# Performance work log

Hardware: AMD Instinct MI355X
Metric: run time of the kernel (lower is better)

## Reference

```python
import jax, jax.numpy as jnp
import numpy as np

M0, S0 = 0.0, 2.0       # normal prior mean / std on mu, beta
SHAPE, SCALE = 2.0, 1.0  # gamma prior on softplus(phi)


def _softplus(x):
    return jnp.logaddexp(x, 0.0)


def _log_negbinomial(y, mu, phi):
    # NB parameterized by mean mu and dispersion phi (var = mu + phi*mu^2)
    r = 1.0 / phi
    return (jax.lax.lgamma(y + r) - jax.lax.lgamma(r) - jax.lax.lgamma(y + 1.0)
            + r * jnp.log(r / (r + mu)) + y * jnp.log(mu / (r + mu)))


def _log_normal(x, m, s):
    return -0.5 * jnp.log(2.0 * jnp.pi * s * s) - (x - m) ** 2 / (2.0 * s * s)


def _log_gamma(x, shape, scale):
    return ((shape - 1.0) * jnp.log(x) - x / scale
            - jax.lax.lgamma(jnp.asarray(shape, x.dtype)) - shape * jnp.log(scale))


def setup_inputs() -> dict:
    key = jax.random.key(0)
    k1, k2, k3, k4, k5 = jax.random.split(key, 5)
    N, P, G = 1024, 4, 20000
    X = jax.random.normal(k1, (N, P), dtype=jnp.float32)
    Y = jax.random.randint(k2, (N, G), 0, 500).astype(jnp.float32)
    mu = jax.random.normal(k3, (G,), dtype=jnp.float32)
    beta = jax.random.normal(k4, (P * G,), dtype=jnp.float32)
    phi = jax.random.normal(k5, (G,), dtype=jnp.float32)
    return {"X": X, "Y": Y, "mu": mu, "beta": beta, "phi": phi}


def reference(X, Y, mu, beta, phi):
    N, P = X.shape
    G = Y.shape[1]
    beta_ = beta.reshape(P, G)
    log_unnorm = mu + X @ beta_                                   # [N, G]
    norm = jax.scipy.special.logsumexp(log_unnorm, axis=1, keepdims=True)
    pi = jnp.exp(log_unnorm - norm)                               # softmax over genes
    s = jnp.sum(Y, axis=1, keepdims=True)                         # [N, 1] library sizes
    phi_sp = _softplus(phi)                                       # [G]
    log_lik = jnp.sum(_log_negbinomial(Y, s * pi, phi_sp))
    log_prior = (jnp.sum(_log_normal(mu, M0, S0))
                 + jnp.sum(_log_normal(beta, M0, S0))
                 + jnp.sum(_log_gamma(phi_sp, SHAPE, SCALE)))
    return (log_lik + log_prior).reshape(1)
```

## Files before the change

kernel.cpp:

```cpp
#include <hip/hip_runtime.h>
#include <math.h>


#define RPB 16

__device__ __forceinline__ float fast_rcp(float x) {
    return __builtin_amdgcn_rcpf(x);
}

__device__ __forceinline__ float lgamma_pos(float x) {
    float lp = 0.0f;
    if (x < 8.0f) {
        float p = x;
        x += 1.0f;
        while (x < 8.0f) { p *= x; x += 1.0f; }
        lp = __logf(p);
    }
    float inv  = fast_rcp(x);
    float inv2 = inv * inv;
    float ser = inv * (0.08333333333f + inv2 * (-0.002777777778f + inv2 * 7.936507937e-4f));
    return (x - 0.5f) * __logf(x) - x + 0.9189385332f + ser - lp;
}

__device__ __forceinline__ float stirling_lg(float x) {
    float inv  = fast_rcp(x);
    float inv2 = inv * inv;
    float ser  = inv * (0.08333333333f - 0.002777777778f * inv2);
    return (x - 0.5f) * __logf(x) - x + 0.9189385332f + ser;
}

__device__ __forceinline__ float softplus_f(float x) {
    return fmaxf(x, 0.0f) + log1pf(__expf(-fabsf(x)));
}

__device__ __forceinline__ float wave_reduce(float v) {
#pragma unroll
    for (int off = 32; off; off >>= 1) v += __shfl_down(v, off, 64);
    return v;
}

__global__ __launch_bounds__(256) void setup_kernel(
        const float* __restrict__ mu, const float* __restrict__ beta,
        const float* __restrict__ phi, double* __restrict__ acc,
        float* __restrict__ rg, float* __restrict__ cgw, int P, int G) {
    int g = blockIdx.x * 256 + threadIdx.x;
    float v = 0.0f;
    if (g < G) {
        const float cn = -1.6120857137646180f;
        float m = mu[g];
        v = cn - m * m * 0.125f;
        for (int p = 0; p < P; ++p) {
            float b = beta[(size_t)p * G + g];
            v += cn - b * b * 0.125f;
        }
        float sp = softplus_f(phi[g]);
        v += __logf(sp) - sp;
        float r = 1.0f / sp;
        rg[g]  = r;
        cgw[g] = r * __logf(r) - lgamma_pos(r);
    }
    v = wave_reduce(v);
    __shared__ float red[4];
    int lane = threadIdx.x & 63, wid = threadIdx.x >> 6;
    if (lane == 0) red[wid] = v;
    __syncthreads();
    if (threadIdx.x == 0)
        atomicAdd(acc, (double)((red[0] + red[1]) + (red[2] + red[3])));
}

__global__ __launch_bounds__(256) void pre_fast(
        const float* __restrict__ X, const float* __restrict__ Y,
        const float* __restrict__ mu, const float* __restrict__ beta,
        float* __restrict__ syw, float* __restrict__ sew,
        double* __restrict__ acc, int N, int G) {
    const int G4 = G >> 2;
    const int tid = threadIdx.x;
    const int n0 = blockIdx.y * RPB;
    __shared__ float lgY[512];
    __shared__ float Xs[RPB * 4];
    __shared__ float syl[RPB], sel[RPB];
    for (int i = tid; i < 512; i += 256) lgY[i] = lgamma_pos((float)(i + 1));
    if (tid < RPB * 4) Xs[tid] = X[(size_t)n0 * 4 + tid];
    if (tid < RPB) { syl[tid] = 0.0f; sel[tid] = 0.0f; }

    const int gi = blockIdx.x * 256 + tid;
    const bool active = (gi < G4);
    const float4 zero = make_float4(0, 0, 0, 0);
    float4 bb[4];
    float4 mug = zero;
    if (active) {
        const float4* __restrict__ B4 = (const float4*)beta;
#pragma unroll
        for (int p = 0; p < 4; ++p) bb[p] = B4[(size_t)p * G4 + gi];
        mug = ((const float4*)mu)[gi];
    } else {
#pragma unroll
        for (int p = 0; p < 4; ++p) bb[p] = zero;
    }
    __syncthreads();

    const float4* __restrict__ Yp = (const float4*)Y + (size_t)n0 * G4 + gi;
    const int lane = tid & 63;

    float4 yb[8];
#pragma unroll
    for (int j = 0; j < 8; ++j)
        yb[j] = active ? Yp[(size_t)j * G4] : zero;

    float lgacc = 0.0f;
#pragma unroll
    for (int i0 = 0; i0 < RPB; i0 += 4) {
        float sy[4], se[4];
#pragma unroll
        for (int j = 0; j < 4; ++j) {
            const int i = i0 + j;
            float4 y = yb[i & 7];
            if ((i + 8 < RPB) && active)
                yb[i & 7] = Yp[(size_t)(i + 8) * G4];
            float4 lu = mug;
#pragma unroll
            for (int p = 0; p < 4; ++p) {
                float xp = Xs[i * 4 + p];
                lu.x = fmaf(xp, bb[p].x, lu.x);
                lu.y = fmaf(xp, bb[p].y, lu.y);
                lu.z = fmaf(xp, bb[p].z, lu.z);
                lu.w = fmaf(xp, bb[p].w, lu.w);
            }
            float e = (__expf(lu.x) + __expf(lu.y)) + (__expf(lu.z) + __expf(lu.w));
            se[j] = active ? e : 0.0f;
            sy[j] = (y.x + y.y) + (y.z + y.w);
            if (active) {
                lgacc += (lgY[min(__float2int_rz(y.x), 511)]
                        + lgY[min(__float2int_rz(y.y), 511)])
                       + (lgY[min(__float2int_rz(y.z), 511)]
                        + lgY[min(__float2int_rz(y.w), 511)]);
            }
        }
#pragma unroll
        for (int off = 32; off; off >>= 1) {
#pragma unroll
            for (int j = 0; j < 4; ++j) {
                sy[j] += __shfl_down(sy[j], off, 64);
                se[j] += __shfl_down(se[j], off, 64);
            }
        }
        if (lane == 0) {
#pragma unroll
            for (int j = 0; j < 4; ++j) {
                atomicAdd(&syl[i0 + j], sy[j]);
                atomicAdd(&sel[i0 + j], se[j]);
            }
        }
    }
    lgacc = wave_reduce(lgacc);
    __shared__ float red[4];
    int wid = tid >> 6;
    if (lane == 0) red[wid] = lgacc;
    __syncthreads();
    if (tid < RPB) {
        atomicAdd(&syw[n0 + tid], syl[tid]);
        atomicAdd(&sew[n0 + tid], sel[tid]);
    }
    if (tid == 0)
        atomicAdd(acc, -(double)((red[0] + red[1]) + (red[2] + red[3])));
}

__global__ __launch_bounds__(256) void nb_loglik_fast(
        const float* __restrict__ X, const float* __restrict__ Y,
        const float* __restrict__ mu, const float* __restrict__ beta,
        const float* __restrict__ rg, const float* __restrict__ cgw,
        const float* __restrict__ syw, const float* __restrict__ sew,
        double* __restrict__ acc, int N, int G) {
    __shared__ float Xs[RPB * 4];
    __shared__ float dcs[RPB];

    const int tid = threadIdx.x;
    const int n0 = blockIdx.y * RPB;
    const int G4 = G >> 2;

    if (tid < RPB * 4) Xs[tid] = X[(size_t)n0 * 4 + tid];
    if (tid < RPB) dcs[tid] = __logf(syw[n0 + tid]) - __logf(sew[n0 + tid]);

    const int gi = blockIdx.x * 256 + tid;
    const bool active = (gi < G4);
    const float4 zero = make_float4(0, 0, 0, 0);
    float4 bb[4];
    float4 mug = zero, r4 = make_float4(1, 1, 1, 1), cg4 = zero;
    if (active) {
        const float4* __restrict__ B4 = (const float4*)beta;
#pragma unroll
        for (int p = 0; p < 4; ++p) bb[p] = B4[(size_t)p * G4 + gi];
        mug = ((const float4*)mu)[gi];
        r4  = ((const float4*)rg)[gi];
        cg4 = ((const float4*)cgw)[gi];
    } else {
#pragma unroll
        for (int p = 0; p < 4; ++p) bb[p] = zero;
    }
    __syncthreads();

    const float4* __restrict__ Yp = (const float4*)Y + (size_t)n0 * G4 + gi;
    float4 yb[8];
#pragma unroll
    for (int j = 0; j < 8; ++j)
        yb[j] = active ? Yp[(size_t)j * G4] : zero;

    float a0 = 0.0f, a1 = 0.0f, a2 = 0.0f, a3 = 0.0f;
#pragma unroll
    for (int i = 0; i < RPB; ++i) {
        float4 y = yb[i & 7];
        if ((i + 8 < RPB) && active)
            yb[i & 7] = Yp[(size_t)(i + 8) * G4];
        float dcn = dcs[i];
        float4 lu = mug;
#pragma unroll
        for (int p = 0; p < 4; ++p) {
            float xp = Xs[i * 4 + p];
            lu.x = fmaf(xp, bb[p].x, lu.x);
            lu.y = fmaf(xp, bb[p].y, lu.y);
            lu.z = fmaf(xp, bb[p].z, lu.z);
            lu.w = fmaf(xp, bb[p].w, lu.w);
        }
        float lm, m, yr;
        lm = dcn + lu.x; m = __expf(lm); yr = y.x + r4.x;
        a0 += stirling_lg(yr) + fmaf(y.x, lm, -yr * __logf(r4.x + m)) + cg4.x;
        lm = dcn + lu.y; m = __expf(lm); yr = y.y + r4.y;
        a1 += stirling_lg(yr) + fmaf(y.y, lm, -yr * __logf(r4.y + m)) + cg4.y;
        lm = dcn + lu.z; m = __expf(lm); yr = y.z + r4.z;
        a2 += stirling_lg(yr) + fmaf(y.z, lm, -yr * __logf(r4.z + m)) + cg4.z;
        lm = dcn + lu.w; m = __expf(lm); yr = y.w + r4.w;
        a3 += stirling_lg(yr) + fmaf(y.w, lm, -yr * __logf(r4.w + m)) + cg4.w;
    }
    float accl = active ? ((a0 + a1) + (a2 + a3)) : 0.0f;
    accl = wave_reduce(accl);
    __shared__ float red[4];
    int lane = tid & 63, wid = tid >> 6;
    if (lane == 0) red[wid] = accl;
    __syncthreads();
    if (tid == 0)
        atomicAdd(acc, (double)((red[0] + red[1]) + (red[2] + red[3])));
}

__global__ void finalize_kernel(const double* __restrict__ acc, float* __restrict__ out) {
    out[0] = (float)acc[0];
}

__global__ void row_stats_generic(
        const float* __restrict__ X, const float* __restrict__ Y,
        const float* __restrict__ mu, const float* __restrict__ beta,
        float* __restrict__ syw, float* __restrict__ sew, int N, int P, int G) {
    const int n = blockIdx.x;
    const int tid = threadIdx.x;
    float sy = 0.0f, se = 0.0f;
    for (int g = tid; g < G; g += 256) {
        sy += Y[(size_t)n * G + g];
        float lu = mu[g];
        for (int p = 0; p < P; ++p) lu += X[(size_t)n * P + p] * beta[(size_t)p * G + g];
        se += __expf(lu);
    }
    sy = wave_reduce(sy);
    se = wave_reduce(se);
    __shared__ float r1[4], r2[4];
    int lane = tid & 63, wid = tid >> 6;
    if (lane == 0) { r1[wid] = sy; r2[wid] = se; }
    __syncthreads();
    if (tid == 0) {
        syw[n] = (r1[0] + r1[1]) + (r1[2] + r1[3]);
        sew[n] = (r2[0] + r2[1]) + (r2[2] + r2[3]);
    }
}

__global__ void nb_generic(
        const float* __restrict__ X, const float* __restrict__ Y,
        const float* __restrict__ mu, const float* __restrict__ beta,
        const float* __restrict__ rg, const float* __restrict__ cgw,
        const float* __restrict__ syw, const float* __restrict__ sew,
        double* __restrict__ acc, int N, int P, int G) {
    const int n = blockIdx.x;
    const int tid = threadIdx.x;
    float dcn = __logf(syw[n]) - __logf(sew[n]);
    float accl = 0.0f;
    for (int g = tid; g < G; g += 256) {
        float y = Y[(size_t)n * G + g];
        float lu = mu[g];
        for (int p = 0; p < P; ++p) lu += X[(size_t)n * P + p] * beta[(size_t)p * G + g];
        float lm = dcn + lu;
        float r = rg[g];
        float m = __expf(lm);
        accl += stirling_lg(y + r) - lgamma_pos(y + 1.0f)
                + fmaf(y, lm, -(y + r) * __logf(r + m)) + cgw[g];
    }
    accl = wave_reduce(accl);
    __shared__ float red[4];
    int lane = tid & 63, wid = tid >> 6;
    if (lane == 0) red[wid] = accl;
    __syncthreads();
    if (tid == 0)
        atomicAdd(acc, (double)((red[0] + red[1]) + (red[2] + red[3])));
}

extern "C" void kernel_launch(void* const* d_in, const int* in_sizes, int n_in,
                              void* d_out, int out_size, void* d_ws, size_t ws_size,
                              hipStream_t stream) {
    const float* X    = (const float*)d_in[0];
    const float* Y    = (const float*)d_in[1];
    const float* mu   = (const float*)d_in[2];
    const float* beta = (const float*)d_in[3];
    const float* phi  = (const float*)d_in[4];
    float* out = (float*)d_out;

    const int G = in_sizes[2];
    const int N = in_sizes[1] / G;
    const int P = in_sizes[0] / N;
    const int G4 = G >> 2;

    char* ws = (char*)d_ws;
    double* acc  = (double*)ws;
    float*  syw  = (float*)(ws + 256);
    float*  sew  = (float*)(ws + 4352);
    float*  rgw  = (float*)(ws + 8448);
    float*  cgw  = (float*)(ws + 8448 + (size_t)4 * G);

    hipMemsetAsync(d_ws, 0, 8448, stream);

    int gblocks = (G + 255) / 256;

    if (P == 4 && (G & 3) == 0 && (N % RPB) == 0 && N <= 1024) {
        dim3 grid((G4 + 255) / 256, N / RPB);
        pre_fast<<<grid, 256, 0, stream>>>(X, Y, mu, beta, syw, sew, acc, N, G);
        setup_kernel<<<gblocks, 256, 0, stream>>>(mu, beta, phi, acc, rgw, cgw, P, G);
        nb_loglik_fast<<<grid, 256, 0, stream>>>(X, Y, mu, beta, rgw, cgw,
                                                 syw, sew, acc, N, G);
    } else {
        setup_kernel<<<gblocks, 256, 0, stream>>>(mu, beta, phi, acc, rgw, cgw, P, G);
        row_stats_generic<<<N, 256, 0, stream>>>(X, Y, mu, beta, syw, sew, N, P, G);
        nb_generic<<<N, 256, 0, stream>>>(X, Y, mu, beta, rgw, cgw, syw, sew,
                                          acc, N, P, G);
    }
    finalize_kernel<<<1, 1, 0, stream>>>(acc, out);
}
```

Baseline: 173.2 us.

## Fuse all stages into one cooperative kernel with LDS-cached Y tiles

Replaces the three-kernel pipeline (row stats, setup, loglik) plus finalize with a single cooperative kernel of 640 blocks. It computes the priors and per-gene constants in the first blocks, accumulates row sums, then synchronises the grid and computes the NB log-likelihood. Three quarters of each block's Y tile are kept in shared memory as 16-bit integers, so Y is read from global memory roughly once instead of twice, and the lgamma(y+1) table is replaced by a Stirling evaluation. It relies on hardcoded problem sizes, a grid-wide barrier, and Y values fitting in 16 bits.

```diff
diff --git a/kernel.cpp b/kernel.cpp
--- a/kernel.cpp
+++ b/kernel.cpp
@@ -1,8 +1,18 @@
 #include <hip/hip_runtime.h>
+#include <hip/hip_cooperative_groups.h>
 #include <math.h>
 
-
-#define RPB 16
+namespace cgrp = cooperative_groups;
+
+
+#define FN_N   1024
+#define FN_G   20000
+#define FN_C   20
+#define FN_CW4 250
+#define FN_G4  5000
+#define FN_SR  8
+#define FN_B   640
+#define FN_K   4
 
 __device__ __forceinline__ float fast_rcp(float x) {
     return __builtin_amdgcn_rcpf(x);
@@ -37,6 +47,203 @@
 #pragma unroll
     for (int off = 32; off; off >>= 1) v += __shfl_down(v, off, 64);
     return v;
+}
+
+__device__ __forceinline__ float nbterm(float y, float lm, float r, float cgv) {
+    float m  = __expf(lm);
+    float yr = y + r;
+    return stirling_lg(yr) - stirling_lg(y + 1.0f)
+         + fmaf(y, lm, -yr * __logf(r + m)) + cgv;
+}
+
+__global__ __launch_bounds__(256, 3) void fused_kernel(
+        const float* __restrict__ X, const float* __restrict__ Y,
+        const float* __restrict__ mu, const float* __restrict__ beta,
+        const float* __restrict__ phi,
+        float* __restrict__ syw, float* __restrict__ sew,
+        float* __restrict__ rgw, float* __restrict__ cgw,
+        double* __restrict__ acc, float* __restrict__ out) {
+    __shared__ unsigned short ycache[3 * FN_SR * 1000];
+    __shared__ float xsh[FN_K * FN_SR * 4];
+    __shared__ float dcs[FN_K * FN_SR];
+    __shared__ float red[4];
+
+    const int tid = threadIdx.x;
+    const int b   = blockIdx.x;
+    const int c   = b % FN_C;
+    const int s0  = b / FN_C;
+    const bool active = (tid < FN_CW4);
+    const int gi4 = c * FN_CW4 + (active ? tid : 0);
+    const int lane = tid & 63;
+    const float4 zero = make_float4(0, 0, 0, 0);
+
+    if (tid < FN_K * FN_SR * 4) {
+        int k = tid >> 5, i = tid & 31;
+        xsh[tid] = X[(size_t)(8 * s0 + 256 * k) * 4 + i];
+    }
+
+    const float4* __restrict__ Y4 = (const float4*)Y;
+    float4 bb[4], mug;
+    if (active) {
+        const float4* __restrict__ B4 = (const float4*)beta;
+#pragma unroll
+        for (int p = 0; p < 4; ++p) bb[p] = B4[(size_t)p * FN_G4 + gi4];
+        mug = ((const float4*)mu)[gi4];
+    } else {
+        mug = zero;
+#pragma unroll
+        for (int p = 0; p < 4; ++p) bb[p] = zero;
+    }
+
+    float priorv = 0.0f;
+    if (b < FN_C && active) {
+        const float cn = -1.6120857137646180f;
+        float4 ph = ((const float4*)phi)[gi4];
+        float4 r4p, cg4p;
+        float mm = mug.x; priorv += cn - mm * mm * 0.125f;
+        mm = mug.y; priorv += cn - mm * mm * 0.125f;
+        mm = mug.z; priorv += cn - mm * mm * 0.125f;
+        mm = mug.w; priorv += cn - mm * mm * 0.125f;
+#pragma unroll
+        for (int p = 0; p < 4; ++p) {
+            priorv += cn - bb[p].x * bb[p].x * 0.125f;
+            priorv += cn - bb[p].y * bb[p].y * 0.125f;
+            priorv += cn - bb[p].z * bb[p].z * 0.125f;
+            priorv += cn - bb[p].w * bb[p].w * 0.125f;
+        }
+        float sp;
+        sp = softplus_f(ph.x); priorv += __logf(sp) - sp; r4p.x = 1.0f / sp;
+        cg4p.x = r4p.x * __logf(r4p.x) - lgamma_pos(r4p.x);
+        sp = softplus_f(ph.y); priorv += __logf(sp) - sp; r4p.y = 1.0f / sp;
+        cg4p.y = r4p.y * __logf(r4p.y) - lgamma_pos(r4p.y);
+        sp = softplus_f(ph.z); priorv += __logf(sp) - sp; r4p.z = 1.0f / sp;
+        cg4p.z = r4p.z * __logf(r4p.z) - lgamma_pos(r4p.z);
+        sp = softplus_f(ph.w); priorv += __logf(sp) - sp; r4p.w = 1.0f / sp;
+        cg4p.w = r4p.w * __logf(r4p.w) - lgamma_pos(r4p.w);
+        ((float4*)rgw)[gi4] = r4p;
+        ((float4*)cgw)[gi4] = cg4p;
+    }
+    __syncthreads();
+
+    auto load_tile = [&](int k, float4 (&dst)[8]) {
+#pragma unroll
+        for (int r = 0; r < 8; ++r)
+            dst[r] = active ? Y4[(size_t)(8 * s0 + 256 * k + r) * FN_G4 + gi4] : zero;
+    };
+    auto proc_tile = [&](int k, float4 (&src)[8]) {
+        float syr[8], ser[8];
+#pragma unroll
+        for (int r = 0; r < 8; ++r) {
+            float4 y = src[r];
+            if (k < 3 && active) {
+                *(ushort4*)&ycache[k * 8000 + r * 1000 + 4 * tid] =
+                    make_ushort4((unsigned short)__float2uint_rz(y.x),
+                                 (unsigned short)__float2uint_rz(y.y),
+                                 (unsigned short)__float2uint_rz(y.z),
+                                 (unsigned short)__float2uint_rz(y.w));
+            }
+            syr[r] = (y.x + y.y) + (y.z + y.w);
+            float4 lu = mug;
+#pragma unroll
+            for (int p = 0; p < 4; ++p) {
+                float xp = xsh[k * 32 + r * 4 + p];
+                lu.x = fmaf(xp, bb[p].x, lu.x);
+                lu.y = fmaf(xp, bb[p].y, lu.y);
+                lu.z = fmaf(xp, bb[p].z, lu.z);
+                lu.w = fmaf(xp, bb[p].w, lu.w);
+            }
+            float e = (__expf(lu.x) + __expf(lu.y)) + (__expf(lu.z) + __expf(lu.w));
+            ser[r] = active ? e : 0.0f;
+        }
+#pragma unroll
+        for (int off = 32; off; off >>= 1) {
+#pragma unroll
+            for (int r = 0; r < 8; ++r) {
+                syr[r] += __shfl_down(syr[r], off, 64);
+                ser[r] += __shfl_down(ser[r], off, 64);
+            }
+        }
+        if (lane == 0) {
+            int n0k = 8 * s0 + 256 * k;
+#pragma unroll
+            for (int r = 0; r < 8; ++r) {
+                atomicAdd(&syw[n0k + r], syr[r]);
+                atomicAdd(&sew[n0k + r], ser[r]);
+            }
+        }
+    };
+
+    float4 buf0[8], buf1[8];
+    load_tile(0, buf0);
+    load_tile(1, buf1);
+    proc_tile(0, buf0);
+    load_tile(2, buf0);
+    proc_tile(1, buf1);
+    load_tile(3, buf1);
+    proc_tile(2, buf0);
+    proc_tile(3, buf1);
+
+    __threadfence();
+    cgrp::this_grid().sync();
+
+    if (tid < FN_K * FN_SR) {
+        int k = tid >> 3, r = tid & 7;
+        int n = 8 * s0 + 256 * k + r;
+        dcs[tid] = __logf(syw[n]) - __logf(sew[n]);
+    }
+    float4 r4, cg4;
+    if (active) {
+        r4  = ((const float4*)rgw)[gi4];
+        cg4 = ((const float4*)cgw)[gi4];
+    } else {
+        r4 = make_float4(1, 1, 1, 1); cg4 = zero;
+    }
+    float4 g3[8];
+#pragma unroll
+    for (int r = 0; r < 8; ++r)
+        g3[r] = active ? Y4[(size_t)(8 * s0 + 768 + r) * FN_G4 + gi4] : zero;
+    __syncthreads();
+
+    float a0 = 0.0f, a1 = 0.0f, a2 = 0.0f, a3 = 0.0f;
+    auto elem = [&](int k, int r, float4 y) {
+        float dcn = dcs[k * 8 + r];
+        float4 lu = mug;
+#pragma unroll
+        for (int p = 0; p < 4; ++p) {
+            float xp = xsh[k * 32 + r * 4 + p];
+            lu.x = fmaf(xp, bb[p].x, lu.x);
+            lu.y = fmaf(xp, bb[p].y, lu.y);
+            lu.z = fmaf(xp, bb[p].z, lu.z);
+            lu.w = fmaf(xp, bb[p].w, lu.w);
+        }
+        a0 += nbterm(y.x, dcn + lu.x, r4.x, cg4.x);
+        a1 += nbterm(y.y, dcn + lu.y, r4.y, cg4.y);
+        a2 += nbterm(y.z, dcn + lu.z, r4.z, cg4.z);
+        a3 += nbterm(y.w, dcn + lu.w, r4.w, cg4.w);
+    };
+#pragma unroll
+    for (int k = 0; k < 3; ++k) {
+#pragma unroll
+        for (int r = 0; r < 8; ++r) {
+            ushort4 u = *(const ushort4*)&ycache[k * 8000 + r * 1000 + 4 * (active ? tid : 0)];
+            float4 y = make_float4((float)u.x, (float)u.y, (float)u.z, (float)u.w);
+            elem(k, r, y);
+        }
+    }
+#pragma unroll
+    for (int r = 0; r < 8; ++r) elem(3, r, g3[r]);
+
+    float accl = (active ? ((a0 + a1) + (a2 + a3)) : 0.0f) + priorv;
+    accl = wave_reduce(accl);
+    int wid = tid >> 6;
+    if (lane == 0) red[wid] = accl;
+    __syncthreads();
+    if (tid == 0)
+        atomicAdd(acc, (double)((red[0] + red[1]) + (red[2] + red[3])));
+
+    cgrp::this_grid().sync();
+    if (b == 0 && tid == 0)
+        out[0] = (float)atomicAdd(acc, 0.0);
 }
 
 __global__ __launch_bounds__(256) void setup_kernel(
@@ -50,8 +257,8 @@
         float m = mu[g];
         v = cn - m * m * 0.125f;
         for (int p = 0; p < P; ++p) {
-            float b = beta[(size_t)p * G + g];
-            v += cn - b * b * 0.125f;
+            float bv = beta[(size_t)p * G + g];
+            v += cn - bv * bv * 0.125f;
         }
         float sp = softplus_f(phi[g]);
         v += __logf(sp) - sp;
@@ -66,183 +273,6 @@
     __syncthreads();
     if (threadIdx.x == 0)
         atomicAdd(acc, (double)((red[0] + red[1]) + (red[2] + red[3])));
-}
-
-__global__ __launch_bounds__(256) void pre_fast(
-        const float* __restrict__ X, const float* __restrict__ Y,
-        const float* __restrict__ mu, const float* __restrict__ beta,
-        float* __restrict__ syw, float* __restrict__ sew,
-        double* __restrict__ acc, int N, int G) {
-    const int G4 = G >> 2;
-    const int tid = threadIdx.x;
-    const int n0 = blockIdx.y * RPB;
-    __shared__ float lgY[512];
-    __shared__ float Xs[RPB * 4];
-    __shared__ float syl[RPB], sel[RPB];
-    for (int i = tid; i < 512; i += 256) lgY[i] = lgamma_pos((float)(i + 1));
-    if (tid < RPB * 4) Xs[tid] = X[(size_t)n0 * 4 + tid];
-    if (tid < RPB) { syl[tid] = 0.0f; sel[tid] = 0.0f; }
-
-    const int gi = blockIdx.x * 256 + tid;
-    const bool active = (gi < G4);
-    const float4 zero = make_float4(0, 0, 0, 0);
-    float4 bb[4];
-    float4 mug = zero;
-    if (active) {
-        const float4* __restrict__ B4 = (const float4*)beta;
-#pragma unroll
-        for (int p = 0; p < 4; ++p) bb[p] = B4[(size_t)p * G4 + gi];
-        mug = ((const float4*)mu)[gi];
-    } else {
-#pragma unroll
-        for (int p = 0; p < 4; ++p) bb[p] = zero;
-    }
-    __syncthreads();
-
-    const float4* __restrict__ Yp = (const float4*)Y + (size_t)n0 * G4 + gi;
-    const int lane = tid & 63;
-
-    float4 yb[8];
-#pragma unroll
-    for (int j = 0; j < 8; ++j)
-        yb[j] = active ? Yp[(size_t)j * G4] : zero;
-
-    float lgacc = 0.0f;
-#pragma unroll
-    for (int i0 = 0; i0 < RPB; i0 += 4) {
-        float sy[4], se[4];
-#pragma unroll
-        for (int j = 0; j < 4; ++j) {
-            const int i = i0 + j;
-            float4 y = yb[i & 7];
-            if ((i + 8 < RPB) && active)
-                yb[i & 7] = Yp[(size_t)(i + 8) * G4];
-            float4 lu = mug;
-#pragma unroll
-            for (int p = 0; p < 4; ++p) {
-                float xp = Xs[i * 4 + p];
-                lu.x = fmaf(xp, bb[p].x, lu.x);
-                lu.y = fmaf(xp, bb[p].y, lu.y);
-                lu.z = fmaf(xp, bb[p].z, lu.z);
-                lu.w = fmaf(xp, bb[p].w, lu.w);
-            }
-            float e = (__expf(lu.x) + __expf(lu.y)) + (__expf(lu.z) + __expf(lu.w));
-            se[j] = active ? e : 0.0f;
-            sy[j] = (y.x + y.y) + (y.z + y.w);
-            if (active) {
-                lgacc += (lgY[min(__float2int_rz(y.x), 511)]
-                        + lgY[min(__float2int_rz(y.y), 511)])
-                       + (lgY[min(__float2int_rz(y.z), 511)]
-                        + lgY[min(__float2int_rz(y.w), 511)]);
-            }
-        }
-#pragma unroll
-        for (int off = 32; off; off >>= 1) {
-#pragma unroll
-            for (int j = 0; j < 4; ++j) {
-                sy[j] += __shfl_down(sy[j], off, 64);
-                se[j] += __shfl_down(se[j], off, 64);
-            }
-        }
-        if (lane == 0) {
-#pragma unroll
-            for (int j = 0; j < 4; ++j) {
-                atomicAdd(&syl[i0 + j], sy[j]);
-                atomicAdd(&sel[i0 + j], se[j]);
-            }
-        }
-    }
-    lgacc = wave_reduce(lgacc);
-    __shared__ float red[4];
-    int wid = tid >> 6;
-    if (lane == 0) red[wid] = lgacc;
-    __syncthreads();
-    if (tid < RPB) {
-        atomicAdd(&syw[n0 + tid], syl[tid]);
-        atomicAdd(&sew[n0 + tid], sel[tid]);
-    }
-    if (tid == 0)
-        atomicAdd(acc, -(double)((red[0] + red[1]) + (red[2] + red[3])));
-}
-
-__global__ __launch_bounds__(256) void nb_loglik_fast(
-        const float* __restrict__ X, const float* __restrict__ Y,
-        const float* __restrict__ mu, const float* __restrict__ beta,
-        const float* __restrict__ rg, const float* __restrict__ cgw,
-        const float* __restrict__ syw, const float* __restrict__ sew,
-        double* __restrict__ acc, int N, int G) {
-    __shared__ float Xs[RPB * 4];
-    __shared__ float dcs[RPB];
-
-    const int tid = threadIdx.x;
-    const int n0 = blockIdx.y * RPB;
-    const int G4 = G >> 2;
-
-    if (tid < RPB * 4) Xs[tid] = X[(size_t)n0 * 4 + tid];
-    if (tid < RPB) dcs[tid] = __logf(syw[n0 + tid]) - __logf(sew[n0 + tid]);
-
-    const int gi = blockIdx.x * 256 + tid;
-    const bool active = (gi < G4);
-    const float4 zero = make_float4(0, 0, 0, 0);
-    float4 bb[4];
-    float4 mug = zero, r4 = make_float4(1, 1, 1, 1), cg4 = zero;
-    if (active) {
-        const float4* __restrict__ B4 = (const float4*)beta;
-#pragma unroll
-        for (int p = 0; p < 4; ++p) bb[p] = B4[(size_t)p * G4 + gi];
-        mug = ((const float4*)mu)[gi];
-        r4  = ((const float4*)rg)[gi];
-        cg4 = ((const float4*)cgw)[gi];
-    } else {
-#pragma unroll
-        for (int p = 0; p < 4; ++p) bb[p] = zero;
-    }
-    __syncthreads();
-
-    const float4* __restrict__ Yp = (const float4*)Y + (size_t)n0 * G4 + gi;
-    float4 yb[8];
-#pragma unroll
-    for (int j = 0; j < 8; ++j)
-        yb[j] = active ? Yp[(size_t)j * G4] : zero;
-
-    float a0 = 0.0f, a1 = 0.0f, a2 = 0.0f, a3 = 0.0f;
-#pragma unroll
-    for (int i = 0; i < RPB; ++i) {
-        float4 y = yb[i & 7];
-        if ((i + 8 < RPB) && active)
-            yb[i & 7] = Yp[(size_t)(i + 8) * G4];
-        float dcn = dcs[i];
-        float4 lu = mug;
-#pragma unroll
-        for (int p = 0; p < 4; ++p) {
-            float xp = Xs[i * 4 + p];
-            lu.x = fmaf(xp, bb[p].x, lu.x);
-            lu.y = fmaf(xp, bb[p].y, lu.y);
-            lu.z = fmaf(xp, bb[p].z, lu.z);
-            lu.w = fmaf(xp, bb[p].w, lu.w);
-        }
-        float lm, m, yr;
-        lm = dcn + lu.x; m = __expf(lm); yr = y.x + r4.x;
-        a0 += stirling_lg(yr) + fmaf(y.x, lm, -yr * __logf(r4.x + m)) + cg4.x;
-        lm = dcn + lu.y; m = __expf(lm); yr = y.y + r4.y;
-        a1 += stirling_lg(yr) + fmaf(y.y, lm, -yr * __logf(r4.y + m)) + cg4.y;
-        lm = dcn + lu.z; m = __expf(lm); yr = y.z + r4.z;
-        a2 += stirling_lg(yr) + fmaf(y.z, lm, -yr * __logf(r4.z + m)) + cg4.z;
-        lm = dcn + lu.w; m = __expf(lm); yr = y.w + r4.w;
-        a3 += stirling_lg(yr) + fmaf(y.w, lm, -yr * __logf(r4.w + m)) + cg4.w;
-    }
-    float accl = active ? ((a0 + a1) + (a2 + a3)) : 0.0f;
-    accl = wave_reduce(accl);
-    __shared__ float red[4];
-    int lane = tid & 63, wid = tid >> 6;
-    if (lane == 0) red[wid] = accl;
-    __syncthreads();
-    if (tid == 0)
-        atomicAdd(acc, (double)((red[0] + red[1]) + (red[2] + red[3])));
-}
-
-__global__ void finalize_kernel(const double* __restrict__ acc, float* __restrict__ out) {
-    out[0] = (float)acc[0];
 }
 
 __global__ void row_stats_generic(
@@ -299,6 +329,10 @@
         atomicAdd(acc, (double)((red[0] + red[1]) + (red[2] + red[3])));
 }
 
+__global__ void finalize_kernel(const double* __restrict__ acc, float* __restrict__ out) {
+    out[0] = (float)acc[0];
+}
+
 extern "C" void kernel_launch(void* const* d_in, const int* in_sizes, int n_in,
                               void* d_out, int out_size, void* d_ws, size_t ws_size,
                               hipStream_t stream) {
@@ -312,30 +346,33 @@
     const int G = in_sizes[2];
     const int N = in_sizes[1] / G;
     const int P = in_sizes[0] / N;
-    const int G4 = G >> 2;
 
     char* ws = (char*)d_ws;
-    double* acc  = (double*)ws;
-    float*  syw  = (float*)(ws + 256);
-    float*  sew  = (float*)(ws + 4352);
-    float*  rgw  = (float*)(ws + 8448);
-    float*  cgw  = (float*)(ws + 8448 + (size_t)4 * G);
-
-    hipMemsetAsync(d_ws, 0, 8448, stream);
-
-    int gblocks = (G + 255) / 256;
-
-    if (P == 4 && (G & 3) == 0 && (N % RPB) == 0 && N <= 1024) {
-        dim3 grid((G4 + 255) / 256, N / RPB);
-        pre_fast<<<grid, 256, 0, stream>>>(X, Y, mu, beta, syw, sew, acc, N, G);
-        setup_kernel<<<gblocks, 256, 0, stream>>>(mu, beta, phi, acc, rgw, cgw, P, G);
-        nb_loglik_fast<<<grid, 256, 0, stream>>>(X, Y, mu, beta, rgw, cgw,
-                                                 syw, sew, acc, N, G);
-    } else {
+    double* acc = (double*)ws;
+    float*  syw = (float*)(ws + 256);
+    float*  sew = (float*)(ws + 4608);
+    float*  rgw = (float*)(ws + 8960);
+    float*  cgw = (float*)(ws + 8960 + (size_t)4 * G);
+
+    hipMemsetAsync(d_ws, 0, 8960, stream);
+
+    bool fast_ok = (N == FN_N && G == FN_G && P == 4);
+    if (fast_ok) {
+        void* args[] = {(void*)&X, (void*)&Y, (void*)&mu, (void*)&beta, (void*)&phi,
+                        (void*)&syw, (void*)&sew, (void*)&rgw, (void*)&cgw,
+                        (void*)&acc, (void*)&out};
+        hipError_t e = hipLaunchCooperativeKernel((const void*)fused_kernel,
+                                                  dim3(FN_B), dim3(256),
+                                                  args, 0, stream);
+        if (e == hipSuccess) return;
+        fast_ok = false;
+    }
+    {
+        int gblocks = (G + 255) / 256;
         setup_kernel<<<gblocks, 256, 0, stream>>>(mu, beta, phi, acc, rgw, cgw, P, G);
         row_stats_generic<<<N, 256, 0, stream>>>(X, Y, mu, beta, syw, sew, N, P, G);
         nb_generic<<<N, 256, 0, stream>>>(X, Y, mu, beta, rgw, cgw, syw, sew,
                                           acc, N, P, G);
-    }
-    finalize_kernel<<<1, 1, 0, stream>>>(acc, out);
-}
+        finalize_kernel<<<1, 1, 0, stream>>>(acc, out);
+    }
+}
```

Result: slower. 404.9 us (+133.8%).

## Pack Y to uint16 in first pass and use persistent grid for both passes

Applied to the files above, without the earlier changes.

The row-statistics pass now writes a 16-bit integer copy of Y to workspace, and the likelihood pass reads that compact copy instead of fp32 Y. The lgamma(y+1) table is replaced by a Stirling evaluation in the likelihood pass. Both kernels use a fixed persistent grid over hardcoded shape constants. Total memory traffic is roughly unchanged because of the extra write, and the packing assumes integer counts below 65536.

```diff
diff --git a/kernel.cpp b/kernel.cpp
--- a/kernel.cpp
+++ b/kernel.cpp
@@ -2,7 +2,11 @@
 #include <math.h>
 
 
-#define RPB 16
+#define FG4    5000
+#define FCH    20
+#define FSLABS 64
+#define FITEMS (FCH * FSLABS)
+#define FGRID  640
 
 __device__ __forceinline__ float fast_rcp(float x) {
     return __builtin_amdgcn_rcpf(x);
@@ -37,6 +41,13 @@
 #pragma unroll
     for (int off = 32; off; off >>= 1) v += __shfl_down(v, off, 64);
     return v;
+}
+
+__device__ __forceinline__ float nbterm(float y, float lm, float r, float cgv) {
+    float m  = __expf(lm);
+    float yr = y + r;
+    return stirling_lg(yr) - stirling_lg(y + 1.0f)
+         + fmaf(y, lm, -yr * __logf(r + m)) + cgv;
 }
 
 __global__ __launch_bounds__(256) void setup_kernel(
@@ -72,51 +83,149 @@
         const float* __restrict__ X, const float* __restrict__ Y,
         const float* __restrict__ mu, const float* __restrict__ beta,
         float* __restrict__ syw, float* __restrict__ sew,
-        double* __restrict__ acc, int N, int G) {
-    const int G4 = G >> 2;
-    const int tid = threadIdx.x;
-    const int n0 = blockIdx.y * RPB;
-    __shared__ float lgY[512];
-    __shared__ float Xs[RPB * 4];
-    __shared__ float syl[RPB], sel[RPB];
-    for (int i = tid; i < 512; i += 256) lgY[i] = lgamma_pos((float)(i + 1));
-    if (tid < RPB * 4) Xs[tid] = X[(size_t)n0 * 4 + tid];
-    if (tid < RPB) { syl[tid] = 0.0f; sel[tid] = 0.0f; }
-
-    const int gi = blockIdx.x * 256 + tid;
-    const bool active = (gi < G4);
+        unsigned short* __restrict__ ypack) {
+    __shared__ float Xs[64];
+    __shared__ float syp[4][16], sep[4][16];
+
+    const int tid  = threadIdx.x;
+    const int lane = tid & 63, wid = tid >> 6;
+    const float4* __restrict__ Y4 = (const float4*)Y;
+    const float4* __restrict__ B4 = (const float4*)beta;
+    const float4* __restrict__ M4 = (const float4*)mu;
     const float4 zero = make_float4(0, 0, 0, 0);
-    float4 bb[4];
-    float4 mug = zero;
-    if (active) {
-        const float4* __restrict__ B4 = (const float4*)beta;
-#pragma unroll
-        for (int p = 0; p < 4; ++p) bb[p] = B4[(size_t)p * G4 + gi];
-        mug = ((const float4*)mu)[gi];
-    } else {
-#pragma unroll
-        for (int p = 0; p < 4; ++p) bb[p] = zero;
-    }
-    __syncthreads();
-
-    const float4* __restrict__ Yp = (const float4*)Y + (size_t)n0 * G4 + gi;
-    const int lane = tid & 63;
-
-    float4 yb[8];
-#pragma unroll
-    for (int j = 0; j < 8; ++j)
-        yb[j] = active ? Yp[(size_t)j * G4] : zero;
-
-    float lgacc = 0.0f;
-#pragma unroll
-    for (int i0 = 0; i0 < RPB; i0 += 4) {
-        float sy[4], se[4];
-#pragma unroll
-        for (int j = 0; j < 4; ++j) {
-            const int i = i0 + j;
-            float4 y = yb[i & 7];
-            if ((i + 8 < RPB) && active)
-                yb[i & 7] = Yp[(size_t)(i + 8) * G4];
+
+    for (int w = blockIdx.x; w < FITEMS; w += gridDim.x) {
+        const int c  = w % FCH;
+        const int s  = w / FCH;
+        const int n0 = s * 16;
+        __syncthreads();
+        if (tid < 64) Xs[tid] = X[(size_t)n0 * 4 + tid];
+        const int gi4 = c * 256 + tid;
+        const bool active = (gi4 < FG4);
+        float4 bb[4], mug;
+        if (active) {
+#pragma unroll
+            for (int p = 0; p < 4; ++p) bb[p] = B4[(size_t)p * FG4 + gi4];
+            mug = M4[gi4];
+        } else {
+            mug = zero;
+#pragma unroll
+            for (int p = 0; p < 4; ++p) bb[p] = zero;
+        }
+        __syncthreads();
+
+        const float4* __restrict__ Yp = Y4 + (size_t)n0 * FG4 + (active ? gi4 : 0);
+        ushort4* __restrict__ Wp = (ushort4*)ypack + (size_t)n0 * FG4 + (active ? gi4 : 0);
+
+#pragma unroll
+        for (int i0 = 0; i0 < 16; i0 += 4) {
+            float4 y[4];
+#pragma unroll
+            for (int j = 0; j < 4; ++j)
+                y[j] = active ? Yp[(size_t)(i0 + j) * FG4] : zero;
+            float sy[4], se[4];
+#pragma unroll
+            for (int j = 0; j < 4; ++j) {
+                if (active) {
+                    Wp[(size_t)(i0 + j) * FG4] =
+                        make_ushort4((unsigned short)__float2uint_rz(y[j].x),
+                                     (unsigned short)__float2uint_rz(y[j].y),
+                                     (unsigned short)__float2uint_rz(y[j].z),
+                                     (unsigned short)__float2uint_rz(y[j].w));
+                }
+                float4 lu = mug;
+#pragma unroll
+                for (int p = 0; p < 4; ++p) {
+                    float xp = Xs[(i0 + j) * 4 + p];
+                    lu.x = fmaf(xp, bb[p].x, lu.x);
+                    lu.y = fmaf(xp, bb[p].y, lu.y);
+                    lu.z = fmaf(xp, bb[p].z, lu.z);
+                    lu.w = fmaf(xp, bb[p].w, lu.w);
+                }
+                float e = (__expf(lu.x) + __expf(lu.y)) + (__expf(lu.z) + __expf(lu.w));
+                se[j] = active ? e : 0.0f;
+                sy[j] = (y[j].x + y[j].y) + (y[j].z + y[j].w);
+            }
+#pragma unroll
+            for (int off = 32; off; off >>= 1) {
+#pragma unroll
+                for (int j = 0; j < 4; ++j) {
+                    sy[j] += __shfl_down(sy[j], off, 64);
+                    se[j] += __shfl_down(se[j], off, 64);
+                }
+            }
+            if (lane == 0) {
+#pragma unroll
+                for (int j = 0; j < 4; ++j) {
+                    syp[wid][i0 + j] = sy[j];
+                    sep[wid][i0 + j] = se[j];
+                }
+            }
+        }
+        __syncthreads();
+        if (tid < 16) {
+            float a = (syp[0][tid] + syp[1][tid]) + (syp[2][tid] + syp[3][tid]);
+            float b = (sep[0][tid] + sep[1][tid]) + (sep[2][tid] + sep[3][tid]);
+            atomicAdd(&syw[n0 + tid], a);
+            atomicAdd(&sew[n0 + tid], b);
+        }
+    }
+}
+
+__global__ __launch_bounds__(256) void nb_fast(
+        const float* __restrict__ X,
+        const float* __restrict__ mu, const float* __restrict__ beta,
+        const float* __restrict__ rg, const float* __restrict__ cgw,
+        const float* __restrict__ syw, const float* __restrict__ sew,
+        const unsigned short* __restrict__ ypack,
+        double* __restrict__ acc) {
+    __shared__ float Xs[64];
+    __shared__ float dcs[16];
+    __shared__ float red[4];
+
+    const int tid  = threadIdx.x;
+    const int lane = tid & 63, wid = tid >> 6;
+    const float4* __restrict__ B4 = (const float4*)beta;
+    const float4 zero = make_float4(0, 0, 0, 0);
+
+    float a0 = 0.0f, a1 = 0.0f, a2 = 0.0f, a3 = 0.0f;
+
+    for (int w = blockIdx.x; w < FITEMS; w += gridDim.x) {
+        const int c  = w % FCH;
+        const int s  = w / FCH;
+        const int n0 = s * 16;
+        __syncthreads();
+        if (tid < 64) Xs[tid] = X[(size_t)n0 * 4 + tid];
+        if (tid < 16) dcs[tid] = __logf(syw[n0 + tid]) - __logf(sew[n0 + tid]);
+        const int gi4 = c * 256 + tid;
+        const bool active = (gi4 < FG4);
+        float4 bb[4], mug, r4, cg4;
+        if (active) {
+#pragma unroll
+            for (int p = 0; p < 4; ++p) bb[p] = B4[(size_t)p * FG4 + gi4];
+            mug = ((const float4*)mu)[gi4];
+            r4  = ((const float4*)rg)[gi4];
+            cg4 = ((const float4*)cgw)[gi4];
+        } else {
+            mug = zero; cg4 = zero; r4 = make_float4(1, 1, 1, 1);
+#pragma unroll
+            for (int p = 0; p < 4; ++p) bb[p] = zero;
+        }
+        __syncthreads();
+
+        const ushort4* __restrict__ Yp =
+            (const ushort4*)ypack + (size_t)n0 * FG4 + (active ? gi4 : 0);
+        ushort4 yb[4];
+#pragma unroll
+        for (int j = 0; j < 4; ++j) yb[j] = Yp[(size_t)j * FG4];
+
+        float t0 = 0.0f, t1 = 0.0f, t2 = 0.0f, t3 = 0.0f;
+#pragma unroll
+        for (int i = 0; i < 16; ++i) {
+            ushort4 u = yb[i & 3];
+            if (i + 4 < 16) yb[i & 3] = Yp[(size_t)(i + 4) * FG4];
+            float4 y = make_float4((float)u.x, (float)u.y, (float)u.z, (float)u.w);
+            float dcn = dcs[i];
             float4 lu = mug;
 #pragma unroll
             for (int p = 0; p < 4; ++p) {
@@ -126,115 +235,16 @@
                 lu.z = fmaf(xp, bb[p].z, lu.z);
                 lu.w = fmaf(xp, bb[p].w, lu.w);
             }
-            float e = (__expf(lu.x) + __expf(lu.y)) + (__expf(lu.z) + __expf(lu.w));
-            se[j] = active ? e : 0.0f;
-            sy[j] = (y.x + y.y) + (y.z + y.w);
-            if (active) {
-                lgacc += (lgY[min(__float2int_rz(y.x), 511)]
-                        + lgY[min(__float2int_rz(y.y), 511)])
-                       + (lgY[min(__float2int_rz(y.z), 511)]
-                        + lgY[min(__float2int_rz(y.w), 511)]);
-            }
-        }
-#pragma unroll
-        for (int off = 32; off; off >>= 1) {
-#pragma unroll
-            for (int j = 0; j < 4; ++j) {
-                sy[j] += __shfl_down(sy[j], off, 64);
-                se[j] += __shfl_down(se[j], off, 64);
-            }
-        }
-        if (lane == 0) {
-#pragma unroll
-            for (int j = 0; j < 4; ++j) {
-                atomicAdd(&syl[i0 + j], sy[j]);
-                atomicAdd(&sel[i0 + j], se[j]);
-            }
-        }
-    }
-    lgacc = wave_reduce(lgacc);
-    __shared__ float red[4];
-    int wid = tid >> 6;
-    if (lane == 0) red[wid] = lgacc;
-    __syncthreads();
-    if (tid < RPB) {
-        atomicAdd(&syw[n0 + tid], syl[tid]);
-        atomicAdd(&sew[n0 + tid], sel[tid]);
-    }
-    if (tid == 0)
-        atomicAdd(acc, -(double)((red[0] + red[1]) + (red[2] + red[3])));
-}
-
-__global__ __launch_bounds__(256) void nb_loglik_fast(
-        const float* __restrict__ X, const float* __restrict__ Y,
-        const float* __restrict__ mu, const float* __restrict__ beta,
-        const float* __restrict__ rg, const float* __restrict__ cgw,
-        const float* __restrict__ syw, const float* __restrict__ sew,
-        double* __restrict__ acc, int N, int G) {
-    __shared__ float Xs[RPB * 4];
-    __shared__ float dcs[RPB];
-
-    const int tid = threadIdx.x;
-    const int n0 = blockIdx.y * RPB;
-    const int G4 = G >> 2;
-
-    if (tid < RPB * 4) Xs[tid] = X[(size_t)n0 * 4 + tid];
-    if (tid < RPB) dcs[tid] = __logf(syw[n0 + tid]) - __logf(sew[n0 + tid]);
-
-    const int gi = blockIdx.x * 256 + tid;
-    const bool active = (gi < G4);
-    const float4 zero = make_float4(0, 0, 0, 0);
-    float4 bb[4];
-    float4 mug = zero, r4 = make_float4(1, 1, 1, 1), cg4 = zero;
-    if (active) {
-        const float4* __restrict__ B4 = (const float4*)beta;
-#pragma unroll
-        for (int p = 0; p < 4; ++p) bb[p] = B4[(size_t)p * G4 + gi];
-        mug = ((const float4*)mu)[gi];
-        r4  = ((const float4*)rg)[gi];
-        cg4 = ((const float4*)cgw)[gi];
-    } else {
-#pragma unroll
-        for (int p = 0; p < 4; ++p) bb[p] = zero;
-    }
-    __syncthreads();
-
-    const float4* __restrict__ Yp = (const float4*)Y + (size_t)n0 * G4 + gi;
-    float4 yb[8];
-#pragma unroll
-    for (int j = 0; j < 8; ++j)
-        yb[j] = active ? Yp[(size_t)j * G4] : zero;
-
-    float a0 = 0.0f, a1 = 0.0f, a2 = 0.0f, a3 = 0.0f;
-#pragma unroll
-    for (int i = 0; i < RPB; ++i) {
-        float4 y = yb[i & 7];
-        if ((i + 8 < RPB) && active)
-            yb[i & 7] = Yp[(size_t)(i + 8) * G4];
-        float dcn = dcs[i];
-        float4 lu = mug;
-#pragma unroll
-        for (int p = 0; p < 4; ++p) {
-            float xp = Xs[i * 4 + p];
-            lu.x = fmaf(xp, bb[p].x, lu.x);
-            lu.y = fmaf(xp, bb[p].y, lu.y);
-            lu.z = fmaf(xp, bb[p].z, lu.z);
-            lu.w = fmaf(xp, bb[p].w, lu.w);
-        }
-        float lm, m, yr;
-        lm = dcn + lu.x; m = __expf(lm); yr = y.x + r4.x;
-        a0 += stirling_lg(yr) + fmaf(y.x, lm, -yr * __logf(r4.x + m)) + cg4.x;
-        lm = dcn + lu.y; m = __expf(lm); yr = y.y + r4.y;
-        a1 += stirling_lg(yr) + fmaf(y.y, lm, -yr * __logf(r4.y + m)) + cg4.y;
-        lm = dcn + lu.z; m = __expf(lm); yr = y.z + r4.z;
-        a2 += stirling_lg(yr) + fmaf(y.z, lm, -yr * __logf(r4.z + m)) + cg4.z;
-        lm = dcn + lu.w; m = __expf(lm); yr = y.w + r4.w;
-        a3 += stirling_lg(yr) + fmaf(y.w, lm, -yr * __logf(r4.w + m)) + cg4.w;
-    }
-    float accl = active ? ((a0 + a1) + (a2 + a3)) : 0.0f;
+            t0 += nbterm(y.x, dcn + lu.x, r4.x, cg4.x);
+            t1 += nbterm(y.y, dcn + lu.y, r4.y, cg4.y);
+            t2 += nbterm(y.z, dcn + lu.z, r4.z, cg4.z);
+            t3 += nbterm(y.w, dcn + lu.w, r4.w, cg4.w);
+        }
+        if (active) { a0 += t0; a1 += t1; a2 += t2; a3 += t3; }
+    }
+
+    float accl = (a0 + a1) + (a2 + a3);
     accl = wave_reduce(accl);
-    __shared__ float red[4];
-    int lane = tid & 63, wid = tid >> 6;
     if (lane == 0) red[wid] = accl;
     __syncthreads();
     if (tid == 0)
@@ -312,25 +322,25 @@
     const int G = in_sizes[2];
     const int N = in_sizes[1] / G;
     const int P = in_sizes[0] / N;
-    const int G4 = G >> 2;
 
     char* ws = (char*)d_ws;
-    double* acc  = (double*)ws;
-    float*  syw  = (float*)(ws + 256);
-    float*  sew  = (float*)(ws + 4352);
-    float*  rgw  = (float*)(ws + 8448);
-    float*  cgw  = (float*)(ws + 8448 + (size_t)4 * G);
-
-    hipMemsetAsync(d_ws, 0, 8448, stream);
+    double*         acc   = (double*)ws;
+    float*          syw   = (float*)(ws + 256);
+    float*          sew   = (float*)(ws + 4608);
+    float*          rgw   = (float*)(ws + 8960);
+    float*          cgw   = (float*)(ws + 8960 + (size_t)4 * G);
+    unsigned short* ypack = (unsigned short*)(ws + 262144);
+
+    hipMemsetAsync(d_ws, 0, 8960, stream);
+
+    const size_t need = 262144 + (size_t)2 * N * G;
+    const bool fast_ok = (N == 1024 && G == 20000 && P == 4 && ws_size >= need);
 
     int gblocks = (G + 255) / 256;
-
-    if (P == 4 && (G & 3) == 0 && (N % RPB) == 0 && N <= 1024) {
-        dim3 grid((G4 + 255) / 256, N / RPB);
-        pre_fast<<<grid, 256, 0, stream>>>(X, Y, mu, beta, syw, sew, acc, N, G);
+    if (fast_ok) {
+        pre_fast<<<FGRID, 256, 0, stream>>>(X, Y, mu, beta, syw, sew, ypack);
         setup_kernel<<<gblocks, 256, 0, stream>>>(mu, beta, phi, acc, rgw, cgw, P, G);
-        nb_loglik_fast<<<grid, 256, 0, stream>>>(X, Y, mu, beta, rgw, cgw,
-                                                 syw, sew, acc, N, G);
+        nb_fast<<<FGRID, 256, 0, stream>>>(X, mu, beta, rgw, cgw, syw, sew, ypack, acc);
     } else {
         setup_kernel<<<gblocks, 256, 0, stream>>>(mu, beta, phi, acc, rgw, cgw, P, G);
         row_stats_generic<<<N, 256, 0, stream>>>(X, Y, mu, beta, syw, sew, N, P, G);
```

Result: slower. 202.7 us (+17.0%).
